# Kernel optimization log

Measured on AMD Instinct MI355X. Metric: run time of the kernel, lower is better.

Reference implementation:

```python
import math
import jax, jax.numpy as jnp
import numpy as np

NUM_EXPERTS = 8
TOP_K = 2
HIDDEN = 1024
INTERMEDIATE = 4096
CAPACITY_FACTOR = 1.0


def setup_inputs() -> dict:
    key = jax.random.key(0)
    k1, k2, k3, k4, k5, k6 = jax.random.split(key, 6)
    T = 8192
    hidden_states = jax.random.normal(k1, (T, HIDDEN), dtype=jnp.float32)
    # router affinities (already softmax-normalized in the real pipeline; uniform here is fine for correctness)
    expert_affinities = jax.random.uniform(k2, (T, NUM_EXPERTS), dtype=jnp.float32)
    expert_index = jax.random.randint(k3, (T, TOP_K), 0, NUM_EXPERTS, dtype=jnp.int32)
    scale = 0.02
    gate_w = jax.random.normal(k4, (NUM_EXPERTS, HIDDEN, INTERMEDIATE), dtype=jnp.float32) * scale
    up_w = jax.random.normal(k5, (NUM_EXPERTS, HIDDEN, INTERMEDIATE), dtype=jnp.float32) * scale
    down_w = jax.random.normal(k6, (NUM_EXPERTS, INTERMEDIATE, HIDDEN), dtype=jnp.float32) * scale
    return {"hidden_states": hidden_states, "expert_affinities": expert_affinities,
            "gate_w": gate_w, "up_w": up_w, "down_w": down_w, "expert_index": expert_index}


def reference(hidden_states, expert_affinities, gate_w, up_w, down_w, expert_index):
    T, H = hidden_states.shape
    E, K = NUM_EXPERTS, TOP_K
    C = min(math.ceil(T * K * CAPACITY_FACTOR / E), T)  # expert capacity (static)

    # top_k-hot expert mask (T, E)
    expert_mask = jax.nn.one_hot(expert_index, E, dtype=jnp.float32).sum(axis=1)
    # 1-indexed position of each token within each expert's queue
    position_in_expert = jnp.cumsum(expert_mask, axis=0)
    # capacity-based token dropping
    expert_mask = jnp.where(position_in_expert > C, 0.0, expert_mask)

    # masked (and L1-normalized) affinities of chosen experts
    aff_masked = jnp.where(expert_mask == 0, 0.0, expert_affinities)
    denom = jnp.maximum(jnp.sum(jnp.abs(aff_masked), axis=1, keepdims=True), 1e-12)
    aff_masked = aff_masked / denom  # normalize_top_k_affinities=True

    # flattened slot index per (token, expert): expert e occupies slots [e*C, (e+1)*C)
    offsets = jnp.arange(E, dtype=jnp.float32) * C
    pos_off = position_in_expert + offsets[None, :]
    pos_off = jnp.where(expert_mask == 0, 0.0, pos_off)

    # (T, K) slot index (1-based; 0 == dropped)
    perm_idx = jnp.take_along_axis(pos_off, expert_index, axis=1).astype(jnp.int32)

    # invert permutation: slot -> token (1-based; slot 0 collects all dropped tokens, then discarded)
    tok_ids = jnp.broadcast_to((jnp.arange(T, dtype=jnp.int32) + 1)[:, None], (T, K)).reshape(-1)
    assign = jnp.zeros(E * C + 1, dtype=jnp.int32).at[perm_idx.reshape(-1)].set(tok_ids)
    assign = assign[1:].reshape(E, C) - 1
    assign = jnp.maximum(assign, 0)          # empty slots read token 0 (output unused)
    perm_idx = jnp.maximum(perm_idx - 1, 0)  # dropped tokens read slot 0 (affinity == 0)

    # gather tokens into per-expert blocks and run grouped GLU MLP
    x_e = hidden_states[assign]  # (E, C, H)
    gate = jax.nn.silu(jnp.einsum('ech,ehi->eci', x_e, gate_w))
    inter = gate * jnp.einsum('ech,ehi->eci', x_e, up_w)  # (E, C, I)
    out_e = jnp.einsum('eci,eih->ech', inter, down_w)      # (E, C, H)
    permuted_output = out_e.reshape(E * C, H)

    # combine: gather each token's top_k expert outputs weighted by masked affinities
    out_k = permuted_output[perm_idx]                                   # (T, K, H)
    aff_k = jnp.take_along_axis(aff_masked, expert_index, axis=1)       # (T, K)
    return jnp.sum(out_k * aff_k[:, :, None], axis=1)
```

## Files before the change

kernel.cpp:

```cpp
#include <hip/hip_runtime.h>
#include <stdint.h>

#define T_TOK 8192
#define HID   1024
#define INTER 4096
#define NE    8
#define TOPK  2
#define CAP   2048
#define EC    (NE * CAP)


typedef __attribute__((ext_vector_type(8))) short bf16x8;
typedef __attribute__((ext_vector_type(4))) float f32x4;

static __device__ __forceinline__ unsigned short f2bf(float f) {
    union { float f; unsigned u; } a; a.f = f;
    unsigned r = a.u + 0x7FFFu + ((a.u >> 16) & 1u);
    return (unsigned short)(r >> 16);
}
static __device__ __forceinline__ float bf2f(unsigned short b) {
    union { unsigned u; float f; } a; a.u = ((unsigned)b) << 16;
    return a.f;
}

static __device__ __forceinline__ void gload(const unsigned short* g, unsigned short* l) {
    __builtin_amdgcn_global_load_lds((__attribute__((address_space(1))) void*)(uintptr_t)g,
                                     (__attribute__((address_space(3))) void*)l, 16, 0, 0);
}

#define BAR() do { asm volatile("" ::: "memory"); __builtin_amdgcn_s_barrier(); asm volatile("" ::: "memory"); } while (0)
#define WAITVM(N) asm volatile("s_waitcnt vmcnt(" #N ")" ::: "memory")

__global__ __launch_bounds__(512) void route_kernel(const int* __restrict__ eidx,
                                                    int* __restrict__ perm,
                                                    int* __restrict__ assign) {
    int tid = threadIdx.x;
    for (int i = tid; i < EC; i += 512) assign[i] = 0;
    __syncthreads();
    int e = tid >> 6;
    int lane = tid & 63;
    const int TPL = T_TOK / 64;
    int t0 = lane * TPL;
    int cnt = 0;
    for (int t = t0; t < t0 + TPL; ++t) {
        int e0 = eidx[t * 2], e1 = eidx[t * 2 + 1];
        cnt += (e0 == e) + (e1 == e);
    }
    int incl = cnt;
    #pragma unroll
    for (int off = 1; off < 64; off <<= 1) {
        int n = __shfl_up(incl, off, 64);
        if (lane >= off) incl += n;
    }
    int run = incl - cnt;
    for (int t = t0; t < t0 + TPL; ++t) {
        int e0 = eidx[t * 2], e1 = eidx[t * 2 + 1];
        int c = (e0 == e) + (e1 == e);
        if (c) {
            run += c;
            int pos = run;
            bool keep = (pos <= CAP);
            int pi = keep ? (pos + e * CAP) : 0;
            if (e0 == e) perm[t * 2]     = pi;
            if (e1 == e) perm[t * 2 + 1] = pi;
            if (keep) assign[pi - 1] = t;
        }
    }
}

__global__ __launch_bounds__(256) void transpose_cvt(const float* __restrict__ in,
                                                     unsigned short* __restrict__ out,
                                                     int R, int Cc) {
    __shared__ unsigned short tile[64][68];
    int e = blockIdx.z;
    const float* inp = in + (size_t)e * R * Cc;
    unsigned short* outp = out + (size_t)e * R * Cc;
    int c0 = blockIdx.x * 64, r0 = blockIdx.y * 64;
    int t = threadIdx.x;
    int x = t & 15;
    int ry = t >> 4;
    #pragma unroll
    for (int j = 0; j < 4; ++j) {
        int row = ry + 16 * j;
        float4 v = *(const float4*)(inp + (size_t)(r0 + row) * Cc + c0 + 4 * x);
        ushort4 o;
        o.x = f2bf(v.x); o.y = f2bf(v.y); o.z = f2bf(v.z); o.w = f2bf(v.w);
        *(ushort4*)&tile[row][4 * x] = o;
    }
    __syncthreads();
    #pragma unroll
    for (int j = 0; j < 4; ++j) {
        int oc = ry + 16 * j;
        ushort4 o;
        o.x = tile[4 * x + 0][oc];
        o.y = tile[4 * x + 1][oc];
        o.z = tile[4 * x + 2][oc];
        o.w = tile[4 * x + 3][oc];
        *(ushort4*)(outp + (size_t)(c0 + oc) * R + r0 + 4 * x) = o;
    }
}

__global__ __launch_bounds__(256) void gather_cvt(const float* __restrict__ hs,
                                                  const int* __restrict__ assign,
                                                  unsigned short* __restrict__ xe) {
    int s = blockIdx.x;
    int tok = assign[s];
    const float* src = hs + (size_t)tok * HID;
    unsigned short* dst = xe + (size_t)s * HID;
    int h = threadIdx.x * 4;
    float4 v = *(const float4*)(src + h);
    ushort4 o;
    o.x = f2bf(v.x); o.y = f2bf(v.y); o.z = f2bf(v.z); o.w = f2bf(v.w);
    *(ushort4*)(dst + h) = o;
}


__global__ __launch_bounds__(512, 2) void gateup_gemm(const unsigned short* __restrict__ Xe,
                                                      const unsigned short* __restrict__ WgT,
                                                      const unsigned short* __restrict__ WuT,
                                                      unsigned short* __restrict__ interB) {
    extern __shared__ __align__(16) unsigned short smemU[];
    const int K = HID;
    const int NT = K / 64;

    int d  = blockIdx.x + 8 * blockIdx.y + 256 * blockIdx.z;
    int e  = d & 7;
    int m0 = ((d >> 3) & 7) * 256;
    int n0 = (d >> 6) * 128;

    int tid = threadIdx.x;
    int lane = tid & 63, w = tid >> 6;
    int lm = lane & 15, hi = lane >> 4;
    int wm = w >> 2, wn = w & 3;

    const int aRd  = (wm * 128 + lm) * 32 + ((hi ^ (lm & 3)) << 3);
    const int bRd0 = (wn * 32 + lm) * 64 + ((hi ^ (lm & 7)) << 3);
    const int bRd1 = (wn * 32 + lm) * 64 + (((4 + hi) ^ (lm & 7)) << 3);

    int sAr = w * 32 + (lane >> 2);
    int sAc = ((lane & 3) ^ ((lane >> 2) & 3)) << 3;
    const unsigned short* aS0 = Xe + ((size_t)e * CAP + m0 + sAr) * K + sAc;
    const unsigned short* aS1 = aS0 + (size_t)16 * K;
    int sBr = w * 16 + (lane >> 3);
    int sBc = ((lane & 7) ^ ((lane >> 3) & 7)) << 3;
    const unsigned short* gS0 = WgT + ((size_t)e * INTER + n0 + sBr) * K + sBc;
    const unsigned short* gS1 = gS0 + (size_t)8 * K;
    const unsigned short* uS0 = WuT + ((size_t)e * INTER + n0 + sBr) * K + sBc;
    const unsigned short* uS1 = uS0 + (size_t)8 * K;

    const int dj0 = (w * 2 + 0) * 512;
    const int dj1 = (w * 2 + 1) * 512;

    f32x4 zero = {0.f, 0.f, 0.f, 0.f};
    f32x4 accG[8][2], accU[8][2];
    #pragma unroll
    for (int i = 0; i < 8; ++i) {
        accG[i][0] = zero; accG[i][1] = zero;
        accU[i][0] = zero; accU[i][1] = zero;
    }

    {
        unsigned short* wr = smemU;
        gload(aS0,      wr + dj0);          gload(aS1,      wr + dj1);
        gload(gS0,      wr + 16384 + dj0);  gload(gS1,      wr + 16384 + dj1);
        gload(uS0,      wr + 24576 + dj0);  gload(uS1,      wr + 24576 + dj1);
        gload(aS0 + 32, wr + 8192 + dj0);   gload(aS1 + 32, wr + 8192 + dj1);
        WAITVM(4);
        BAR();
    }

    bf16x8 aF[8];

    for (int t = 0; t < NT - 1; ++t) {
        const unsigned short* rd = smemU + (t & 1) * 32768;
        unsigned short* wr = smemU + ((t + 1) & 1) * 32768;
        const int gk = (t + 1) * 64;
        #pragma unroll
        for (int mi = 0; mi < 8; ++mi) aF[mi] = *(const bf16x8*)(rd + aRd + mi * 512);
        bf16x8 b0 = *(const bf16x8*)(rd + 16384 + bRd0);
        bf16x8 b1 = *(const bf16x8*)(rd + 16384 + bRd0 + 1024);
        gload(aS0 + gk, wr + dj0);          gload(aS1 + gk, wr + dj1);
        gload(gS0 + gk, wr + 16384 + dj0);  gload(gS1 + gk, wr + 16384 + dj1);
        WAITVM(6);
        BAR();
        __builtin_amdgcn_s_setprio(1);
        #pragma unroll
        for (int mi = 0; mi < 8; ++mi) {
            accG[mi][0] = __builtin_amdgcn_mfma_f32_16x16x32_bf16(aF[mi], b0, accG[mi][0], 0, 0, 0);
            accG[mi][1] = __builtin_amdgcn_mfma_f32_16x16x32_bf16(aF[mi], b1, accG[mi][1], 0, 0, 0);
        }
        __builtin_amdgcn_s_setprio(0);
        BAR();
        b0 = *(const bf16x8*)(rd + 24576 + bRd0);
        b1 = *(const bf16x8*)(rd + 24576 + bRd0 + 1024);
        gload(uS0 + gk, wr + 24576 + dj0);  gload(uS1 + gk, wr + 24576 + dj1);
        WAITVM(6);
        BAR();
        __builtin_amdgcn_s_setprio(1);
        #pragma unroll
        for (int mi = 0; mi < 8; ++mi) {
            accU[mi][0] = __builtin_amdgcn_mfma_f32_16x16x32_bf16(aF[mi], b0, accU[mi][0], 0, 0, 0);
            accU[mi][1] = __builtin_amdgcn_mfma_f32_16x16x32_bf16(aF[mi], b1, accU[mi][1], 0, 0, 0);
        }
        __builtin_amdgcn_s_setprio(0);
        BAR();
        #pragma unroll
        for (int mi = 0; mi < 8; ++mi) aF[mi] = *(const bf16x8*)(rd + 8192 + aRd + mi * 512);
        b0 = *(const bf16x8*)(rd + 16384 + bRd1);
        b1 = *(const bf16x8*)(rd + 16384 + bRd1 + 1024);
        gload(aS0 + gk + 32, wr + 8192 + dj0);  gload(aS1 + gk + 32, wr + 8192 + dj1);
        BAR();
        __builtin_amdgcn_s_setprio(1);
        #pragma unroll
        for (int mi = 0; mi < 8; ++mi) {
            accG[mi][0] = __builtin_amdgcn_mfma_f32_16x16x32_bf16(aF[mi], b0, accG[mi][0], 0, 0, 0);
            accG[mi][1] = __builtin_amdgcn_mfma_f32_16x16x32_bf16(aF[mi], b1, accG[mi][1], 0, 0, 0);
        }
        __builtin_amdgcn_s_setprio(0);
        BAR();
        b0 = *(const bf16x8*)(rd + 24576 + bRd1);
        b1 = *(const bf16x8*)(rd + 24576 + bRd1 + 1024);
        WAITVM(4);
        BAR();
        __builtin_amdgcn_s_setprio(1);
        #pragma unroll
        for (int mi = 0; mi < 8; ++mi) {
            accU[mi][0] = __builtin_amdgcn_mfma_f32_16x16x32_bf16(aF[mi], b0, accU[mi][0], 0, 0, 0);
            accU[mi][1] = __builtin_amdgcn_mfma_f32_16x16x32_bf16(aF[mi], b1, accU[mi][1], 0, 0, 0);
        }
        __builtin_amdgcn_s_setprio(0);
        BAR();
    }
    {
        const unsigned short* rd = smemU + ((NT - 1) & 1) * 32768;
        #pragma unroll
        for (int mi = 0; mi < 8; ++mi) aF[mi] = *(const bf16x8*)(rd + aRd + mi * 512);
        bf16x8 b0 = *(const bf16x8*)(rd + 16384 + bRd0);
        bf16x8 b1 = *(const bf16x8*)(rd + 16384 + bRd0 + 1024);
        WAITVM(2);
        BAR();
        #pragma unroll
        for (int mi = 0; mi < 8; ++mi) {
            accG[mi][0] = __builtin_amdgcn_mfma_f32_16x16x32_bf16(aF[mi], b0, accG[mi][0], 0, 0, 0);
            accG[mi][1] = __builtin_amdgcn_mfma_f32_16x16x32_bf16(aF[mi], b1, accG[mi][1], 0, 0, 0);
        }
        BAR();
        b0 = *(const bf16x8*)(rd + 24576 + bRd0);
        b1 = *(const bf16x8*)(rd + 24576 + bRd0 + 1024);
        WAITVM(0);
        BAR();
        #pragma unroll
        for (int mi = 0; mi < 8; ++mi) {
            accU[mi][0] = __builtin_amdgcn_mfma_f32_16x16x32_bf16(aF[mi], b0, accU[mi][0], 0, 0, 0);
            accU[mi][1] = __builtin_amdgcn_mfma_f32_16x16x32_bf16(aF[mi], b1, accU[mi][1], 0, 0, 0);
        }
        BAR();
        #pragma unroll
        for (int mi = 0; mi < 8; ++mi) aF[mi] = *(const bf16x8*)(rd + 8192 + aRd + mi * 512);
        b0 = *(const bf16x8*)(rd + 16384 + bRd1);
        b1 = *(const bf16x8*)(rd + 16384 + bRd1 + 1024);
        BAR();
        #pragma unroll
        for (int mi = 0; mi < 8; ++mi) {
            accG[mi][0] = __builtin_amdgcn_mfma_f32_16x16x32_bf16(aF[mi], b0, accG[mi][0], 0, 0, 0);
            accG[mi][1] = __builtin_amdgcn_mfma_f32_16x16x32_bf16(aF[mi], b1, accG[mi][1], 0, 0, 0);
        }
        BAR();
        b0 = *(const bf16x8*)(rd + 24576 + bRd1);
        b1 = *(const bf16x8*)(rd + 24576 + bRd1 + 1024);
        BAR();
        #pragma unroll
        for (int mi = 0; mi < 8; ++mi) {
            accU[mi][0] = __builtin_amdgcn_mfma_f32_16x16x32_bf16(aF[mi], b0, accU[mi][0], 0, 0, 0);
            accU[mi][1] = __builtin_amdgcn_mfma_f32_16x16x32_bf16(aF[mi], b1, accU[mi][1], 0, 0, 0);
        }
        BAR();
    }

    unsigned short* bounce = smemU;
    #pragma unroll
    for (int mi = 0; mi < 8; ++mi)
        #pragma unroll
        for (int nf = 0; nf < 2; ++nf) {
            f32x4 g4 = accG[mi][nf], u4 = accU[mi][nf];
            #pragma unroll
            for (int r = 0; r < 4; ++r) {
                int row = wm * 128 + mi * 16 + hi * 4 + r;
                int col = wn * 32 + nf * 16 + lm;
                float g = g4[r];
                float s = g / (1.f + __expf(-g)) * u4[r];
                bounce[row * 136 + col] = f2bf(s);
            }
        }
    __syncthreads();
    {
        unsigned short* Op = interB + ((size_t)e * CAP + m0) * INTER + n0;
        int rr = tid >> 1, cb = (tid & 1) * 64;
        #pragma unroll
        for (int j = 0; j < 8; ++j) {
            bf16x8 v = *(const bf16x8*)&bounce[rr * 136 + cb + j * 8];
            *(bf16x8*)(Op + (size_t)rr * INTER + cb + j * 8) = v;
        }
    }
}

__global__ __launch_bounds__(512, 2) void down_gemm(const unsigned short* __restrict__ interB,
                                                    const unsigned short* __restrict__ WdT,
                                                    unsigned short* __restrict__ pout) {
    extern __shared__ __align__(16) unsigned short smemU[];
    const int K = INTER;
    const int NT = K / 64;

    int d  = blockIdx.x + 8 * blockIdx.y + 32 * blockIdx.z;
    int e  = d & 7;
    int r5 = d >> 3;
    int m0 = (r5 & 7) * 256;
    int n0 = (r5 >> 3) * 256;

    int tid = threadIdx.x;
    int lane = tid & 63, w = tid >> 6;
    int lm = lane & 15, hi = lane >> 4;
    int wm = w >> 2, wn = w & 3;

    const int aRd  = (wm * 128 + lm) * 32 + ((hi ^ (lm & 3)) << 3);
    const int bRd0 = (wn * 32 + lm) * 64 + ((hi ^ (lm & 7)) << 3);
    const int bRd1 = (wn * 32 + lm) * 64 + (((4 + hi) ^ (lm & 7)) << 3);

    int sAr = w * 32 + (lane >> 2);
    int sAc = ((lane & 3) ^ ((lane >> 2) & 3)) << 3;
    const unsigned short* aS0 = interB + ((size_t)e * CAP + m0 + sAr) * K + sAc;
    const unsigned short* aS1 = aS0 + (size_t)16 * K;
    int sBr = w * 16 + (lane >> 3);
    int sBc = ((lane & 7) ^ ((lane >> 3) & 7)) << 3;
    const unsigned short* b0S0 = WdT + ((size_t)e * HID + n0 + sBr) * K + sBc;
    const unsigned short* b0S1 = b0S0 + (size_t)8 * K;
    const unsigned short* b1S0 = b0S0 + (size_t)128 * K;
    const unsigned short* b1S1 = b1S0 + (size_t)8 * K;

    const int dj0 = (w * 2 + 0) * 512;
    const int dj1 = (w * 2 + 1) * 512;

    f32x4 zero = {0.f, 0.f, 0.f, 0.f};
    f32x4 acc[8][4];
    #pragma unroll
    for (int i = 0; i < 8; ++i)
        #pragma unroll
        for (int j = 0; j < 4; ++j) acc[i][j] = zero;

    {
        unsigned short* wr = smemU;
        gload(aS0,      wr + dj0);          gload(aS1,      wr + dj1);
        gload(b0S0,     wr + 16384 + dj0);  gload(b0S1,     wr + 16384 + dj1);
        gload(b1S0,     wr + 24576 + dj0);  gload(b1S1,     wr + 24576 + dj1);
        gload(aS0 + 32, wr + 8192 + dj0);   gload(aS1 + 32, wr + 8192 + dj1);
        WAITVM(4);
        BAR();
    }

    bf16x8 aF[8];

    for (int t = 0; t < NT - 1; ++t) {
        const unsigned short* rd = smemU + (t & 1) * 32768;
        unsigned short* wr = smemU + ((t + 1) & 1) * 32768;
        const int gk = (t + 1) * 64;
        #pragma unroll
        for (int mi = 0; mi < 8; ++mi) aF[mi] = *(const bf16x8*)(rd + aRd + mi * 512);
        bf16x8 b0 = *(const bf16x8*)(rd + 16384 + bRd0);
        bf16x8 b1 = *(const bf16x8*)(rd + 16384 + bRd0 + 1024);
        gload(aS0 + gk, wr + dj0);           gload(aS1 + gk, wr + dj1);
        gload(b0S0 + gk, wr + 16384 + dj0);  gload(b0S1 + gk, wr + 16384 + dj1);
        WAITVM(6);
        BAR();
        __builtin_amdgcn_s_setprio(1);
        #pragma unroll
        for (int mi = 0; mi < 8; ++mi) {
            acc[mi][0] = __builtin_amdgcn_mfma_f32_16x16x32_bf16(aF[mi], b0, acc[mi][0], 0, 0, 0);
            acc[mi][1] = __builtin_amdgcn_mfma_f32_16x16x32_bf16(aF[mi], b1, acc[mi][1], 0, 0, 0);
        }
        __builtin_amdgcn_s_setprio(0);
        BAR();
        b0 = *(const bf16x8*)(rd + 24576 + bRd0);
        b1 = *(const bf16x8*)(rd + 24576 + bRd0 + 1024);
        gload(b1S0 + gk, wr + 24576 + dj0);  gload(b1S1 + gk, wr + 24576 + dj1);
        WAITVM(6);
        BAR();
        __builtin_amdgcn_s_setprio(1);
        #pragma unroll
        for (int mi = 0; mi < 8; ++mi) {
            acc[mi][2] = __builtin_amdgcn_mfma_f32_16x16x32_bf16(aF[mi], b0, acc[mi][2], 0, 0, 0);
            acc[mi][3] = __builtin_amdgcn_mfma_f32_16x16x32_bf16(aF[mi], b1, acc[mi][3], 0, 0, 0);
        }
        __builtin_amdgcn_s_setprio(0);
        BAR();
        #pragma unroll
        for (int mi = 0; mi < 8; ++mi) aF[mi] = *(const bf16x8*)(rd + 8192 + aRd + mi * 512);
        b0 = *(const bf16x8*)(rd + 16384 + bRd1);
        b1 = *(const bf16x8*)(rd + 16384 + bRd1 + 1024);
        gload(aS0 + gk + 32, wr + 8192 + dj0);  gload(aS1 + gk + 32, wr + 8192 + dj1);
        BAR();
        __builtin_amdgcn_s_setprio(1);
        #pragma unroll
        for (int mi = 0; mi < 8; ++mi) {
            acc[mi][0] = __builtin_amdgcn_mfma_f32_16x16x32_bf16(aF[mi], b0, acc[mi][0], 0, 0, 0);
            acc[mi][1] = __builtin_amdgcn_mfma_f32_16x16x32_bf16(aF[mi], b1, acc[mi][1], 0, 0, 0);
        }
        __builtin_amdgcn_s_setprio(0);
        BAR();
        b0 = *(const bf16x8*)(rd + 24576 + bRd1);
        b1 = *(const bf16x8*)(rd + 24576 + bRd1 + 1024);
        WAITVM(4);
        BAR();
        __builtin_amdgcn_s_setprio(1);
        #pragma unroll
        for (int mi = 0; mi < 8; ++mi) {
            acc[mi][2] = __builtin_amdgcn_mfma_f32_16x16x32_bf16(aF[mi], b0, acc[mi][2], 0, 0, 0);
            acc[mi][3] = __builtin_amdgcn_mfma_f32_16x16x32_bf16(aF[mi], b1, acc[mi][3], 0, 0, 0);
        }
        __builtin_amdgcn_s_setprio(0);
        BAR();
    }
    {
        const unsigned short* rd = smemU + ((NT - 1) & 1) * 32768;
        #pragma unroll
        for (int mi = 0; mi < 8; ++mi) aF[mi] = *(const bf16x8*)(rd + aRd + mi * 512);
        bf16x8 b0 = *(const bf16x8*)(rd + 16384 + bRd0);
        bf16x8 b1 = *(const bf16x8*)(rd + 16384 + bRd0 + 1024);
        WAITVM(2);
        BAR();
        #pragma unroll
        for (int mi = 0; mi < 8; ++mi) {
            acc[mi][0] = __builtin_amdgcn_mfma_f32_16x16x32_bf16(aF[mi], b0, acc[mi][0], 0, 0, 0);
            acc[mi][1] = __builtin_amdgcn_mfma_f32_16x16x32_bf16(aF[mi], b1, acc[mi][1], 0, 0, 0);
        }
        BAR();
        b0 = *(const bf16x8*)(rd + 24576 + bRd0);
        b1 = *(const bf16x8*)(rd + 24576 + bRd0 + 1024);
        WAITVM(0);
        BAR();
        #pragma unroll
        for (int mi = 0; mi < 8; ++mi) {
            acc[mi][2] = __builtin_amdgcn_mfma_f32_16x16x32_bf16(aF[mi], b0, acc[mi][2], 0, 0, 0);
            acc[mi][3] = __builtin_amdgcn_mfma_f32_16x16x32_bf16(aF[mi], b1, acc[mi][3], 0, 0, 0);
        }
        BAR();
        #pragma unroll
        for (int mi = 0; mi < 8; ++mi) aF[mi] = *(const bf16x8*)(rd + 8192 + aRd + mi * 512);
        b0 = *(const bf16x8*)(rd + 16384 + bRd1);
        b1 = *(const bf16x8*)(rd + 16384 + bRd1 + 1024);
        BAR();
        #pragma unroll
        for (int mi = 0; mi < 8; ++mi) {
            acc[mi][0] = __builtin_amdgcn_mfma_f32_16x16x32_bf16(aF[mi], b0, acc[mi][0], 0, 0, 0);
            acc[mi][1] = __builtin_amdgcn_mfma_f32_16x16x32_bf16(aF[mi], b1, acc[mi][1], 0, 0, 0);
        }
        BAR();
        b0 = *(const bf16x8*)(rd + 24576 + bRd1);
        b1 = *(const bf16x8*)(rd + 24576 + bRd1 + 1024);
        BAR();
        #pragma unroll
        for (int mi = 0; mi < 8; ++mi) {
            acc[mi][2] = __builtin_amdgcn_mfma_f32_16x16x32_bf16(aF[mi], b0, acc[mi][2], 0, 0, 0);
            acc[mi][3] = __builtin_amdgcn_mfma_f32_16x16x32_bf16(aF[mi], b1, acc[mi][3], 0, 0, 0);
        }
        BAR();
    }

    unsigned short* bounce = smemU;
    int rr = tid >> 1, cb = (tid & 1) * 64;
    #pragma unroll
    for (int mi = 0; mi < 8; ++mi)
        #pragma unroll
        for (int nfh = 0; nfh < 2; ++nfh) {
            f32x4 a4 = acc[mi][nfh];
            #pragma unroll
            for (int r = 0; r < 4; ++r)
                bounce[(wm * 128 + mi * 16 + hi * 4 + r) * 136 + wn * 32 + nfh * 16 + lm] = f2bf(a4[r]);
        }
    __syncthreads();
    {
        unsigned short* Op = pout + ((size_t)e * CAP + m0) * HID + n0;
        #pragma unroll
        for (int j = 0; j < 8; ++j) {
            bf16x8 v = *(const bf16x8*)&bounce[rr * 136 + cb + j * 8];
            *(bf16x8*)(Op + (size_t)rr * HID + cb + j * 8) = v;
        }
    }
    __syncthreads();
    #pragma unroll
    for (int mi = 0; mi < 8; ++mi)
        #pragma unroll
        for (int nfh = 0; nfh < 2; ++nfh) {
            f32x4 a4 = acc[mi][2 + nfh];
            #pragma unroll
            for (int r = 0; r < 4; ++r)
                bounce[(wm * 128 + mi * 16 + hi * 4 + r) * 136 + wn * 32 + nfh * 16 + lm] = f2bf(a4[r]);
        }
    __syncthreads();
    {
        unsigned short* Op = pout + ((size_t)e * CAP + m0) * HID + n0 + 128;
        #pragma unroll
        for (int j = 0; j < 8; ++j) {
            bf16x8 v = *(const bf16x8*)&bounce[rr * 136 + cb + j * 8];
            *(bf16x8*)(Op + (size_t)rr * HID + cb + j * 8) = v;
        }
    }
}

__global__ __launch_bounds__(256) void combine_kernel(const float* __restrict__ aff,
                                                      const int* __restrict__ eidx,
                                                      const int* __restrict__ perm,
                                                      const unsigned short* __restrict__ pout,
                                                      float* __restrict__ out) {
    int t = blockIdx.x;
    int e0 = eidx[t * 2], e1 = eidx[t * 2 + 1];
    int p0 = perm[t * 2], p1 = perm[t * 2 + 1];
    bool k0 = p0 > 0, k1 = p1 > 0;
    float a0 = aff[t * NE + e0], a1 = aff[t * NE + e1];
    float denom = (k0 ? fabsf(a0) : 0.f) + ((e1 != e0 && k1) ? fabsf(a1) : 0.f);
    denom = fmaxf(denom, 1e-12f);
    float w0 = k0 ? a0 / denom : 0.f;
    float w1 = k1 ? a1 / denom : 0.f;
    int s0 = k0 ? p0 - 1 : 0;
    int s1 = k1 ? p1 - 1 : 0;
    int h = threadIdx.x * 4;
    ushort4 v0 = *(const ushort4*)(pout + (size_t)s0 * HID + h);
    ushort4 v1 = *(const ushort4*)(pout + (size_t)s1 * HID + h);
    float4 o;
    o.x = w0 * bf2f(v0.x) + w1 * bf2f(v1.x);
    o.y = w0 * bf2f(v0.y) + w1 * bf2f(v1.y);
    o.z = w0 * bf2f(v0.z) + w1 * bf2f(v1.z);
    o.w = w0 * bf2f(v0.w) + w1 * bf2f(v1.w);
    *(float4*)(out + (size_t)t * HID + h) = o;
}

extern "C" void kernel_launch(void* const* d_in, const int* in_sizes, int n_in,
                              void* d_out, int out_size, void* d_ws, size_t ws_size,
                              hipStream_t stream) {
    const float* hs   = (const float*)d_in[0];
    const float* aff  = (const float*)d_in[1];
    const float* gw   = (const float*)d_in[2];
    const float* uw   = (const float*)d_in[3];
    const float* dw   = (const float*)d_in[4];
    const int*   eidx = (const int*)d_in[5];
    float* out = (float*)d_out;

    char* ws = (char*)d_ws;
    unsigned short* WgT    = (unsigned short*)(ws);
    unsigned short* WuT    = (unsigned short*)(ws + ((size_t)64  << 20));
    unsigned short* WdT    = (unsigned short*)(ws + ((size_t)128 << 20));
    unsigned short* Xe     = (unsigned short*)(ws + ((size_t)192 << 20));
    unsigned short* interB = (unsigned short*)(ws + ((size_t)224 << 20));
    unsigned short* pout   = (unsigned short*)(ws + ((size_t)352 << 20));
    int*            perm   = (int*)           (ws + ((size_t)416 << 20));
    int*            assign = perm + (T_TOK * TOPK);

    static int attr_set = 0;
    if (!attr_set) {
        (void)hipFuncSetAttribute((const void*)gateup_gemm,
                                  hipFuncAttributeMaxDynamicSharedMemorySize, 131072);
        (void)hipFuncSetAttribute((const void*)down_gemm,
                                  hipFuncAttributeMaxDynamicSharedMemorySize, 131072);
        attr_set = 1;
    }

    route_kernel<<<1, 512, 0, stream>>>(eidx, perm, assign);
    transpose_cvt<<<dim3(INTER / 64, HID / 64, NE), 256, 0, stream>>>(uw, WuT, HID, INTER);
    transpose_cvt<<<dim3(INTER / 64, HID / 64, NE), 256, 0, stream>>>(gw, WgT, HID, INTER);
    gather_cvt<<<EC, 256, 0, stream>>>(hs, assign, Xe);
    gateup_gemm<<<dim3(8, 32, 8), 512, 131072, stream>>>(Xe, WgT, WuT, interB);
    transpose_cvt<<<dim3(HID / 64, INTER / 64, NE), 256, 0, stream>>>(dw, WdT, INTER, HID);
    down_gemm<<<dim3(8, 4, 8), 512, 131072, stream>>>(interB, WdT, pout);
    combine_kernel<<<T_TOK, 256, 0, stream>>>(aff, eidx, perm, pout, out);
}
```

Measured before the change: 936.1 us.

## Restructure grouped GEMMs to 256-thread blocks with triple-buffered K=32 pipeline

Both the gate/up and down GEMMs move from 512-thread blocks with double-buffered K=64 stages to 256-thread blocks with smaller N tiles and a three-stage K=32 ring buffer. This cuts shared memory per block so more blocks can be resident, and keeps more loads in flight. The gate and up weight transposes are merged into a single launch, and the down-weight transpose moves ahead of the gate/up GEMM. In exchange, each block does more loop iterations with more barriers, and the smaller tiles give less reuse of loaded data.

```diff
diff --git a/kernel.cpp b/kernel.cpp
--- a/kernel.cpp
+++ b/kernel.cpp
@@ -68,6 +68,43 @@
     }
 }
 
+__global__ __launch_bounds__(256) void transpose_cvt2(const float* __restrict__ in0,
+                                                      unsigned short* __restrict__ out0,
+                                                      const float* __restrict__ in1,
+                                                      unsigned short* __restrict__ out1) {
+    __shared__ unsigned short tile[64][68];
+    int z = blockIdx.z;
+    const float* in = (z < 8) ? in0 : in1;
+    unsigned short* out = (z < 8) ? out0 : out1;
+    int e = z & 7;
+    const int R = HID, Cc = INTER;
+    const float* inp = in + (size_t)e * R * Cc;
+    unsigned short* outp = out + (size_t)e * R * Cc;
+    int c0 = blockIdx.x * 64, r0 = blockIdx.y * 64;
+    int t = threadIdx.x;
+    int x = t & 15;
+    int ry = t >> 4;
+    #pragma unroll
+    for (int j = 0; j < 4; ++j) {
+        int row = ry + 16 * j;
+        float4 v = *(const float4*)(inp + (size_t)(r0 + row) * Cc + c0 + 4 * x);
+        ushort4 o;
+        o.x = f2bf(v.x); o.y = f2bf(v.y); o.z = f2bf(v.z); o.w = f2bf(v.w);
+        *(ushort4*)&tile[row][4 * x] = o;
+    }
+    __syncthreads();
+    #pragma unroll
+    for (int j = 0; j < 4; ++j) {
+        int oc = ry + 16 * j;
+        ushort4 o;
+        o.x = tile[4 * x + 0][oc];
+        o.y = tile[4 * x + 1][oc];
+        o.z = tile[4 * x + 2][oc];
+        o.w = tile[4 * x + 3][oc];
+        *(ushort4*)(outp + (size_t)(c0 + oc) * R + r0 + 4 * x) = o;
+    }
+}
+
 __global__ __launch_bounds__(256) void transpose_cvt(const float* __restrict__ in,
                                                      unsigned short* __restrict__ out,
                                                      int R, int Cc) {
@@ -115,41 +152,49 @@
 }
 
 
-__global__ __launch_bounds__(512, 2) void gateup_gemm(const unsigned short* __restrict__ Xe,
+#define BUFE 12288
+
+#define MFMA16(ACC, O, B0, B1) \
+    _Pragma("unroll") \
+    for (int mi = 0; mi < 8; ++mi) { \
+        ACC[mi][O]     = __builtin_amdgcn_mfma_f32_16x16x32_bf16(aF[mi], B0, ACC[mi][O], 0, 0, 0); \
+        ACC[mi][O + 1] = __builtin_amdgcn_mfma_f32_16x16x32_bf16(aF[mi], B1, ACC[mi][O + 1], 0, 0, 0); \
+    }
+
+#define LOAD_AF(rd) \
+    _Pragma("unroll") \
+    for (int mi = 0; mi < 8; ++mi) aF[mi] = *(const bf16x8*)((rd) + aRd + mi * 512);
+
+__global__ __launch_bounds__(256, 2) void gateup_gemm(const unsigned short* __restrict__ Xe,
                                                       const unsigned short* __restrict__ WgT,
                                                       const unsigned short* __restrict__ WuT,
                                                       unsigned short* __restrict__ interB) {
     extern __shared__ __align__(16) unsigned short smemU[];
     const int K = HID;
-    const int NT = K / 64;
-
-    int d  = blockIdx.x + 8 * blockIdx.y + 256 * blockIdx.z;
-    int e  = d & 7;
-    int m0 = ((d >> 3) & 7) * 256;
-    int n0 = (d >> 6) * 128;
+    const int NT = K / 32;
+
+    int e  = blockIdx.x;
+    int m0 = blockIdx.y * 256;
+    int n0 = blockIdx.z * 64;
 
     int tid = threadIdx.x;
     int lane = tid & 63, w = tid >> 6;
     int lm = lane & 15, hi = lane >> 4;
-    int wm = w >> 2, wn = w & 3;
-
-    const int aRd  = (wm * 128 + lm) * 32 + ((hi ^ (lm & 3)) << 3);
-    const int bRd0 = (wn * 32 + lm) * 64 + ((hi ^ (lm & 7)) << 3);
-    const int bRd1 = (wn * 32 + lm) * 64 + (((4 + hi) ^ (lm & 7)) << 3);
-
-    int sAr = w * 32 + (lane >> 2);
-    int sAc = ((lane & 3) ^ ((lane >> 2) & 3)) << 3;
-    const unsigned short* aS0 = Xe + ((size_t)e * CAP + m0 + sAr) * K + sAc;
-    const unsigned short* aS1 = aS0 + (size_t)16 * K;
-    int sBr = w * 16 + (lane >> 3);
-    int sBc = ((lane & 7) ^ ((lane >> 3) & 7)) << 3;
-    const unsigned short* gS0 = WgT + ((size_t)e * INTER + n0 + sBr) * K + sBc;
-    const unsigned short* gS1 = gS0 + (size_t)8 * K;
-    const unsigned short* uS0 = WuT + ((size_t)e * INTER + n0 + sBr) * K + sBc;
-    const unsigned short* uS1 = uS0 + (size_t)8 * K;
-
-    const int dj0 = (w * 2 + 0) * 512;
-    const int dj1 = (w * 2 + 1) * 512;
+    int wm = w >> 1, wn = w & 1;
+
+    const int swz  = (hi ^ ((lm >> 1) & 3)) << 3;
+    const int aRd  = (wm * 128 + lm) * 32 + swz;
+    const int r1Rd = 8192  + (wn * 32 + lm) * 32 + swz;
+    const int r2Rd = 10240 + (wn * 32 + lm) * 32 + swz;
+
+    int sr = lane >> 2;
+    int sc = ((lane & 3) ^ ((lane >> 3) & 3)) << 3;
+    const unsigned short* aS = Xe  + ((size_t)e * CAP   + m0 + w * 64 + sr) * K + sc;
+    const unsigned short* gS = WgT + ((size_t)e * INTER + n0 + w * 16 + sr) * K + sc;
+    const unsigned short* uS = WuT + ((size_t)e * INTER + n0 + w * 16 + sr) * K + sc;
+    const int dA = w * 2048;
+    const int dG = 8192  + w * 512;
+    const int dU = 10240 + w * 512;
 
     f32x4 zero = {0.f, 0.f, 0.f, 0.f};
     f32x4 accG[8][2], accU[8][2];
@@ -159,124 +204,81 @@
         accU[i][0] = zero; accU[i][1] = zero;
     }
 
-    {
-        unsigned short* wr = smemU;
-        gload(aS0,      wr + dj0);          gload(aS1,      wr + dj1);
-        gload(gS0,      wr + 16384 + dj0);  gload(gS1,      wr + 16384 + dj1);
-        gload(uS0,      wr + 24576 + dj0);  gload(uS1,      wr + 24576 + dj1);
-        gload(aS0 + 32, wr + 8192 + dj0);   gload(aS1 + 32, wr + 8192 + dj1);
-        WAITVM(4);
+    unsigned short* p0 = smemU;
+    unsigned short* p1 = smemU + BUFE;
+    unsigned short* p2 = smemU + 2 * BUFE;
+
+    {
+        #pragma unroll
+        for (int j = 0; j < 4; ++j) gload(aS + (size_t)j * 16 * K, p0 + dA + j * 512);
+        gload(gS, p0 + dG); gload(uS, p0 + dU);
+        #pragma unroll
+        for (int j = 0; j < 4; ++j) gload(aS + (size_t)j * 16 * K + 32, p1 + dA + j * 512);
+        gload(gS + 32, p1 + dG); gload(uS + 32, p1 + dU);
+        WAITVM(7);
         BAR();
     }
 
     bf16x8 aF[8];
-
-    for (int t = 0; t < NT - 1; ++t) {
-        const unsigned short* rd = smemU + (t & 1) * 32768;
-        unsigned short* wr = smemU + ((t + 1) & 1) * 32768;
-        const int gk = (t + 1) * 64;
-        #pragma unroll
-        for (int mi = 0; mi < 8; ++mi) aF[mi] = *(const bf16x8*)(rd + aRd + mi * 512);
-        bf16x8 b0 = *(const bf16x8*)(rd + 16384 + bRd0);
-        bf16x8 b1 = *(const bf16x8*)(rd + 16384 + bRd0 + 1024);
-        gload(aS0 + gk, wr + dj0);          gload(aS1 + gk, wr + dj1);
-        gload(gS0 + gk, wr + 16384 + dj0);  gload(gS1 + gk, wr + 16384 + dj1);
+    int gk = 64;
+    for (int t = 0; t < NT - 2; ++t) {
+        const unsigned short* rd = p0;
+        unsigned short* wr = p2;
+        LOAD_AF(rd);
+        bf16x8 b0 = *(const bf16x8*)(rd + r1Rd);
+        bf16x8 b1 = *(const bf16x8*)(rd + r1Rd + 512);
+        #pragma unroll
+        for (int j = 0; j < 4; ++j) gload(aS + (size_t)j * 16 * K + gk, wr + dA + j * 512);
+        gload(gS + gk, wr + dG);
+        WAITVM(11);
+        BAR();
+        __builtin_amdgcn_s_setprio(1);
+        MFMA16(accG, 0, b0, b1);
+        __builtin_amdgcn_s_setprio(0);
+        BAR();
+        b0 = *(const bf16x8*)(rd + r2Rd);
+        b1 = *(const bf16x8*)(rd + r2Rd + 512);
+        gload(uS + gk, wr + dU);
+        WAITVM(7);
+        BAR();
+        __builtin_amdgcn_s_setprio(1);
+        MFMA16(accU, 0, b0, b1);
+        __builtin_amdgcn_s_setprio(0);
+        BAR();
+        unsigned short* tmp = p0; p0 = p1; p1 = p2; p2 = tmp;
+        gk += 32;
+    }
+    {
+        const unsigned short* rd = p0;
+        LOAD_AF(rd);
+        bf16x8 b0 = *(const bf16x8*)(rd + r1Rd);
+        bf16x8 b1 = *(const bf16x8*)(rd + r1Rd + 512);
         WAITVM(6);
         BAR();
-        __builtin_amdgcn_s_setprio(1);
-        #pragma unroll
-        for (int mi = 0; mi < 8; ++mi) {
-            accG[mi][0] = __builtin_amdgcn_mfma_f32_16x16x32_bf16(aF[mi], b0, accG[mi][0], 0, 0, 0);
-            accG[mi][1] = __builtin_amdgcn_mfma_f32_16x16x32_bf16(aF[mi], b1, accG[mi][1], 0, 0, 0);
-        }
-        __builtin_amdgcn_s_setprio(0);
-        BAR();
-        b0 = *(const bf16x8*)(rd + 24576 + bRd0);
-        b1 = *(const bf16x8*)(rd + 24576 + bRd0 + 1024);
-        gload(uS0 + gk, wr + 24576 + dj0);  gload(uS1 + gk, wr + 24576 + dj1);
-        WAITVM(6);
-        BAR();
-        __builtin_amdgcn_s_setprio(1);
-        #pragma unroll
-        for (int mi = 0; mi < 8; ++mi) {
-            accU[mi][0] = __builtin_amdgcn_mfma_f32_16x16x32_bf16(aF[mi], b0, accU[mi][0], 0, 0, 0);
-            accU[mi][1] = __builtin_amdgcn_mfma_f32_16x16x32_bf16(aF[mi], b1, accU[mi][1], 0, 0, 0);
-        }
-        __builtin_amdgcn_s_setprio(0);
-        BAR();
-        #pragma unroll
-        for (int mi = 0; mi < 8; ++mi) aF[mi] = *(const bf16x8*)(rd + 8192 + aRd + mi * 512);
-        b0 = *(const bf16x8*)(rd + 16384 + bRd1);
-        b1 = *(const bf16x8*)(rd + 16384 + bRd1 + 1024);
-        gload(aS0 + gk + 32, wr + 8192 + dj0);  gload(aS1 + gk + 32, wr + 8192 + dj1);
-        BAR();
-        __builtin_amdgcn_s_setprio(1);
-        #pragma unroll
-        for (int mi = 0; mi < 8; ++mi) {
-            accG[mi][0] = __builtin_amdgcn_mfma_f32_16x16x32_bf16(aF[mi], b0, accG[mi][0], 0, 0, 0);
-            accG[mi][1] = __builtin_amdgcn_mfma_f32_16x16x32_bf16(aF[mi], b1, accG[mi][1], 0, 0, 0);
-        }
-        __builtin_amdgcn_s_setprio(0);
-        BAR();
-        b0 = *(const bf16x8*)(rd + 24576 + bRd1);
-        b1 = *(const bf16x8*)(rd + 24576 + bRd1 + 1024);
-        WAITVM(4);
-        BAR();
-        __builtin_amdgcn_s_setprio(1);
-        #pragma unroll
-        for (int mi = 0; mi < 8; ++mi) {
-            accU[mi][0] = __builtin_amdgcn_mfma_f32_16x16x32_bf16(aF[mi], b0, accU[mi][0], 0, 0, 0);
-            accU[mi][1] = __builtin_amdgcn_mfma_f32_16x16x32_bf16(aF[mi], b1, accU[mi][1], 0, 0, 0);
-        }
-        __builtin_amdgcn_s_setprio(0);
-        BAR();
-    }
-    {
-        const unsigned short* rd = smemU + ((NT - 1) & 1) * 32768;
-        #pragma unroll
-        for (int mi = 0; mi < 8; ++mi) aF[mi] = *(const bf16x8*)(rd + aRd + mi * 512);
-        bf16x8 b0 = *(const bf16x8*)(rd + 16384 + bRd0);
-        bf16x8 b1 = *(const bf16x8*)(rd + 16384 + bRd0 + 1024);
-        WAITVM(2);
-        BAR();
-        #pragma unroll
-        for (int mi = 0; mi < 8; ++mi) {
-            accG[mi][0] = __builtin_amdgcn_mfma_f32_16x16x32_bf16(aF[mi], b0, accG[mi][0], 0, 0, 0);
-            accG[mi][1] = __builtin_amdgcn_mfma_f32_16x16x32_bf16(aF[mi], b1, accG[mi][1], 0, 0, 0);
-        }
-        BAR();
-        b0 = *(const bf16x8*)(rd + 24576 + bRd0);
-        b1 = *(const bf16x8*)(rd + 24576 + bRd0 + 1024);
+        MFMA16(accG, 0, b0, b1);
+        BAR();
+        b0 = *(const bf16x8*)(rd + r2Rd);
+        b1 = *(const bf16x8*)(rd + r2Rd + 512);
+        WAITVM(1);
+        BAR();
+        MFMA16(accU, 0, b0, b1);
+        BAR();
+    }
+    {
+        const unsigned short* rd = p1;
+        LOAD_AF(rd);
+        bf16x8 b0 = *(const bf16x8*)(rd + r1Rd);
+        bf16x8 b1 = *(const bf16x8*)(rd + r1Rd + 512);
         WAITVM(0);
         BAR();
-        #pragma unroll
-        for (int mi = 0; mi < 8; ++mi) {
-            accU[mi][0] = __builtin_amdgcn_mfma_f32_16x16x32_bf16(aF[mi], b0, accU[mi][0], 0, 0, 0);
-            accU[mi][1] = __builtin_amdgcn_mfma_f32_16x16x32_bf16(aF[mi], b1, accU[mi][1], 0, 0, 0);
-        }
-        BAR();
-        #pragma unroll
-        for (int mi = 0; mi < 8; ++mi) aF[mi] = *(const bf16x8*)(rd + 8192 + aRd + mi * 512);
-        b0 = *(const bf16x8*)(rd + 16384 + bRd1);
-        b1 = *(const bf16x8*)(rd + 16384 + bRd1 + 1024);
-        BAR();
-        #pragma unroll
-        for (int mi = 0; mi < 8; ++mi) {
-            accG[mi][0] = __builtin_amdgcn_mfma_f32_16x16x32_bf16(aF[mi], b0, accG[mi][0], 0, 0, 0);
-            accG[mi][1] = __builtin_amdgcn_mfma_f32_16x16x32_bf16(aF[mi], b1, accG[mi][1], 0, 0, 0);
-        }
-        BAR();
-        b0 = *(const bf16x8*)(rd + 24576 + bRd1);
-        b1 = *(const bf16x8*)(rd + 24576 + bRd1 + 1024);
-        BAR();
-        #pragma unroll
-        for (int mi = 0; mi < 8; ++mi) {
-            accU[mi][0] = __builtin_amdgcn_mfma_f32_16x16x32_bf16(aF[mi], b0, accU[mi][0], 0, 0, 0);
-            accU[mi][1] = __builtin_amdgcn_mfma_f32_16x16x32_bf16(aF[mi], b1, accU[mi][1], 0, 0, 0);
-        }
-        BAR();
-    }
-
+        MFMA16(accG, 0, b0, b1);
+        BAR();
+        b0 = *(const bf16x8*)(rd + r2Rd);
+        b1 = *(const bf16x8*)(rd + r2Rd + 512);
+        MFMA16(accU, 0, b0, b1);
+    }
+
+    __syncthreads();
     unsigned short* bounce = smemU;
     #pragma unroll
     for (int mi = 0; mi < 8; ++mi)
@@ -289,56 +291,52 @@
                 int col = wn * 32 + nf * 16 + lm;
                 float g = g4[r];
                 float s = g / (1.f + __expf(-g)) * u4[r];
-                bounce[row * 136 + col] = f2bf(s);
+                bounce[row * 72 + col] = f2bf(s);
             }
         }
     __syncthreads();
     {
         unsigned short* Op = interB + ((size_t)e * CAP + m0) * INTER + n0;
-        int rr = tid >> 1, cb = (tid & 1) * 64;
+        int rr = tid >> 3, cc = (tid & 7) * 8;
         #pragma unroll
         for (int j = 0; j < 8; ++j) {
-            bf16x8 v = *(const bf16x8*)&bounce[rr * 136 + cb + j * 8];
-            *(bf16x8*)(Op + (size_t)rr * INTER + cb + j * 8) = v;
+            int row = rr + 32 * j;
+            bf16x8 v = *(const bf16x8*)&bounce[row * 72 + cc];
+            *(bf16x8*)(Op + (size_t)row * INTER + cc) = v;
         }
     }
 }
 
-__global__ __launch_bounds__(512, 2) void down_gemm(const unsigned short* __restrict__ interB,
+__global__ __launch_bounds__(256, 2) void down_gemm(const unsigned short* __restrict__ interB,
                                                     const unsigned short* __restrict__ WdT,
                                                     unsigned short* __restrict__ pout) {
     extern __shared__ __align__(16) unsigned short smemU[];
     const int K = INTER;
-    const int NT = K / 64;
-
-    int d  = blockIdx.x + 8 * blockIdx.y + 32 * blockIdx.z;
-    int e  = d & 7;
-    int r5 = d >> 3;
-    int m0 = (r5 & 7) * 256;
-    int n0 = (r5 >> 3) * 256;
+    const int NT = K / 32;
+
+    int e  = blockIdx.x;
+    int m0 = blockIdx.y * 256;
+    int n0 = blockIdx.z * 128;
 
     int tid = threadIdx.x;
     int lane = tid & 63, w = tid >> 6;
     int lm = lane & 15, hi = lane >> 4;
-    int wm = w >> 2, wn = w & 3;
-
-    const int aRd  = (wm * 128 + lm) * 32 + ((hi ^ (lm & 3)) << 3);
-    const int bRd0 = (wn * 32 + lm) * 64 + ((hi ^ (lm & 7)) << 3);
-    const int bRd1 = (wn * 32 + lm) * 64 + (((4 + hi) ^ (lm & 7)) << 3);
-
-    int sAr = w * 32 + (lane >> 2);
-    int sAc = ((lane & 3) ^ ((lane >> 2) & 3)) << 3;
-    const unsigned short* aS0 = interB + ((size_t)e * CAP + m0 + sAr) * K + sAc;
-    const unsigned short* aS1 = aS0 + (size_t)16 * K;
-    int sBr = w * 16 + (lane >> 3);
-    int sBc = ((lane & 7) ^ ((lane >> 3) & 7)) << 3;
-    const unsigned short* b0S0 = WdT + ((size_t)e * HID + n0 + sBr) * K + sBc;
-    const unsigned short* b0S1 = b0S0 + (size_t)8 * K;
-    const unsigned short* b1S0 = b0S0 + (size_t)128 * K;
-    const unsigned short* b1S1 = b1S0 + (size_t)8 * K;
-
-    const int dj0 = (w * 2 + 0) * 512;
-    const int dj1 = (w * 2 + 1) * 512;
+    int wm = w >> 1, wn = w & 1;
+
+    const int swz  = (hi ^ ((lm >> 1) & 3)) << 3;
+    const int aRd  = (wm * 128 + lm) * 32 + swz;
+    const int r1Rd = 8192  + (wn * 32 + lm) * 32 + swz;
+    const int r2Rd = 10240 + (wn * 32 + lm) * 32 + swz;
+
+    int sr = lane >> 2;
+    int sc = ((lane & 3) ^ ((lane >> 3) & 3)) << 3;
+    const unsigned short* aS = interB + ((size_t)e * CAP + m0 + w * 64 + sr) * K + sc;
+    int rb1 = (w >> 1) * 64 + (w & 1) * 16;
+    const unsigned short* b1S = WdT + ((size_t)e * HID + n0 + rb1 + sr) * K + sc;
+    const unsigned short* b2S = WdT + ((size_t)e * HID + n0 + rb1 + 32 + sr) * K + sc;
+    const int dA = w * 2048;
+    const int d1 = 8192  + w * 512;
+    const int d2 = 10240 + w * 512;
 
     f32x4 zero = {0.f, 0.f, 0.f, 0.f};
     f32x4 acc[8][4];
@@ -347,161 +345,106 @@
         #pragma unroll
         for (int j = 0; j < 4; ++j) acc[i][j] = zero;
 
-    {
-        unsigned short* wr = smemU;
-        gload(aS0,      wr + dj0);          gload(aS1,      wr + dj1);
-        gload(b0S0,     wr + 16384 + dj0);  gload(b0S1,     wr + 16384 + dj1);
-        gload(b1S0,     wr + 24576 + dj0);  gload(b1S1,     wr + 24576 + dj1);
-        gload(aS0 + 32, wr + 8192 + dj0);   gload(aS1 + 32, wr + 8192 + dj1);
-        WAITVM(4);
+    unsigned short* p0 = smemU;
+    unsigned short* p1 = smemU + BUFE;
+    unsigned short* p2 = smemU + 2 * BUFE;
+
+    {
+        #pragma unroll
+        for (int j = 0; j < 4; ++j) gload(aS + (size_t)j * 16 * K, p0 + dA + j * 512);
+        gload(b1S, p0 + d1); gload(b2S, p0 + d2);
+        #pragma unroll
+        for (int j = 0; j < 4; ++j) gload(aS + (size_t)j * 16 * K + 32, p1 + dA + j * 512);
+        gload(b1S + 32, p1 + d1); gload(b2S + 32, p1 + d2);
+        WAITVM(7);
         BAR();
     }
 
     bf16x8 aF[8];
-
-    for (int t = 0; t < NT - 1; ++t) {
-        const unsigned short* rd = smemU + (t & 1) * 32768;
-        unsigned short* wr = smemU + ((t + 1) & 1) * 32768;
-        const int gk = (t + 1) * 64;
-        #pragma unroll
-        for (int mi = 0; mi < 8; ++mi) aF[mi] = *(const bf16x8*)(rd + aRd + mi * 512);
-        bf16x8 b0 = *(const bf16x8*)(rd + 16384 + bRd0);
-        bf16x8 b1 = *(const bf16x8*)(rd + 16384 + bRd0 + 1024);
-        gload(aS0 + gk, wr + dj0);           gload(aS1 + gk, wr + dj1);
-        gload(b0S0 + gk, wr + 16384 + dj0);  gload(b0S1 + gk, wr + 16384 + dj1);
+    int gk = 64;
+    for (int t = 0; t < NT - 2; ++t) {
+        const unsigned short* rd = p0;
+        unsigned short* wr = p2;
+        LOAD_AF(rd);
+        bf16x8 b0 = *(const bf16x8*)(rd + r1Rd);
+        bf16x8 b1 = *(const bf16x8*)(rd + r1Rd + 512);
+        #pragma unroll
+        for (int j = 0; j < 4; ++j) gload(aS + (size_t)j * 16 * K + gk, wr + dA + j * 512);
+        gload(b1S + gk, wr + d1);
+        WAITVM(11);
+        BAR();
+        __builtin_amdgcn_s_setprio(1);
+        MFMA16(acc, 0, b0, b1);
+        __builtin_amdgcn_s_setprio(0);
+        BAR();
+        b0 = *(const bf16x8*)(rd + r2Rd);
+        b1 = *(const bf16x8*)(rd + r2Rd + 512);
+        gload(b2S + gk, wr + d2);
+        WAITVM(7);
+        BAR();
+        __builtin_amdgcn_s_setprio(1);
+        MFMA16(acc, 2, b0, b1);
+        __builtin_amdgcn_s_setprio(0);
+        BAR();
+        unsigned short* tmp = p0; p0 = p1; p1 = p2; p2 = tmp;
+        gk += 32;
+    }
+    {
+        const unsigned short* rd = p0;
+        LOAD_AF(rd);
+        bf16x8 b0 = *(const bf16x8*)(rd + r1Rd);
+        bf16x8 b1 = *(const bf16x8*)(rd + r1Rd + 512);
         WAITVM(6);
         BAR();
-        __builtin_amdgcn_s_setprio(1);
-        #pragma unroll
-        for (int mi = 0; mi < 8; ++mi) {
-            acc[mi][0] = __builtin_amdgcn_mfma_f32_16x16x32_bf16(aF[mi], b0, acc[mi][0], 0, 0, 0);
-            acc[mi][1] = __builtin_amdgcn_mfma_f32_16x16x32_bf16(aF[mi], b1, acc[mi][1], 0, 0, 0);
-        }
-        __builtin_amdgcn_s_setprio(0);
-        BAR();
-        b0 = *(const bf16x8*)(rd + 24576 + bRd0);
-        b1 = *(const bf16x8*)(rd + 24576 + bRd0 + 1024);
-        gload(b1S0 + gk, wr + 24576 + dj0);  gload(b1S1 + gk, wr + 24576 + dj1);
-        WAITVM(6);
-        BAR();
-        __builtin_amdgcn_s_setprio(1);
-        #pragma unroll
-        for (int mi = 0; mi < 8; ++mi) {
-            acc[mi][2] = __builtin_amdgcn_mfma_f32_16x16x32_bf16(aF[mi], b0, acc[mi][2], 0, 0, 0);
-            acc[mi][3] = __builtin_amdgcn_mfma_f32_16x16x32_bf16(aF[mi], b1, acc[mi][3], 0, 0, 0);
-        }
-        __builtin_amdgcn_s_setprio(0);
-        BAR();
-        #pragma unroll
-        for (int mi = 0; mi < 8; ++mi) aF[mi] = *(const bf16x8*)(rd + 8192 + aRd + mi * 512);
-        b0 = *(const bf16x8*)(rd + 16384 + bRd1);
-        b1 = *(const bf16x8*)(rd + 16384 + bRd1 + 1024);
-        gload(aS0 + gk + 32, wr + 8192 + dj0);  gload(aS1 + gk + 32, wr + 8192 + dj1);
-        BAR();
-        __builtin_amdgcn_s_setprio(1);
-        #pragma unroll
-        for (int mi = 0; mi < 8; ++mi) {
-            acc[mi][0] = __builtin_amdgcn_mfma_f32_16x16x32_bf16(aF[mi], b0, acc[mi][0], 0, 0, 0);
-            acc[mi][1] = __builtin_amdgcn_mfma_f32_16x16x32_bf16(aF[mi], b1, acc[mi][1], 0, 0, 0);
-        }
-        __builtin_amdgcn_s_setprio(0);
-        BAR();
-        b0 = *(const bf16x8*)(rd + 24576 + bRd1);
-        b1 = *(const bf16x8*)(rd + 24576 + bRd1 + 1024);
-        WAITVM(4);
-        BAR();
-        __builtin_amdgcn_s_setprio(1);
-        #pragma unroll
-        for (int mi = 0; mi < 8; ++mi) {
-            acc[mi][2] = __builtin_amdgcn_mfma_f32_16x16x32_bf16(aF[mi], b0, acc[mi][2], 0, 0, 0);
-            acc[mi][3] = __builtin_amdgcn_mfma_f32_16x16x32_bf16(aF[mi], b1, acc[mi][3], 0, 0, 0);
-        }
-        __builtin_amdgcn_s_setprio(0);
-        BAR();
-    }
-    {
-        const unsigned short* rd = smemU + ((NT - 1) & 1) * 32768;
-        #pragma unroll
-        for (int mi = 0; mi < 8; ++mi) aF[mi] = *(const bf16x8*)(rd + aRd + mi * 512);
-        bf16x8 b0 = *(const bf16x8*)(rd + 16384 + bRd0);
-        bf16x8 b1 = *(const bf16x8*)(rd + 16384 + bRd0 + 1024);
-        WAITVM(2);
-        BAR();
-        #pragma unroll
-        for (int mi = 0; mi < 8; ++mi) {
-            acc[mi][0] = __builtin_amdgcn_mfma_f32_16x16x32_bf16(aF[mi], b0, acc[mi][0], 0, 0, 0);
-            acc[mi][1] = __builtin_amdgcn_mfma_f32_16x16x32_bf16(aF[mi], b1, acc[mi][1], 0, 0, 0);
-        }
-        BAR();
-        b0 = *(const bf16x8*)(rd + 24576 + bRd0);
-        b1 = *(const bf16x8*)(rd + 24576 + bRd0 + 1024);
+        MFMA16(acc, 0, b0, b1);
+        BAR();
+        b0 = *(const bf16x8*)(rd + r2Rd);
+        b1 = *(const bf16x8*)(rd + r2Rd + 512);
+        WAITVM(1);
+        BAR();
+        MFMA16(acc, 2, b0, b1);
+        BAR();
+    }
+    {
+        const unsigned short* rd = p1;
+        LOAD_AF(rd);
+        bf16x8 b0 = *(const bf16x8*)(rd + r1Rd);
+        bf16x8 b1 = *(const bf16x8*)(rd + r1Rd + 512);
         WAITVM(0);
         BAR();
-        #pragma unroll
-        for (int mi = 0; mi < 8; ++mi) {
-            acc[mi][2] = __builtin_amdgcn_mfma_f32_16x16x32_bf16(aF[mi], b0, acc[mi][2], 0, 0, 0);
-            acc[mi][3] = __builtin_amdgcn_mfma_f32_16x16x32_bf16(aF[mi], b1, acc[mi][3], 0, 0, 0);
-        }
-        BAR();
-        #pragma unroll
-        for (int mi = 0; mi < 8; ++mi) aF[mi] = *(const bf16x8*)(rd + 8192 + aRd + mi * 512);
-        b0 = *(const bf16x8*)(rd + 16384 + bRd1);
-        b1 = *(const bf16x8*)(rd + 16384 + bRd1 + 1024);
-        BAR();
-        #pragma unroll
-        for (int mi = 0; mi < 8; ++mi) {
-            acc[mi][0] = __builtin_amdgcn_mfma_f32_16x16x32_bf16(aF[mi], b0, acc[mi][0], 0, 0, 0);
-            acc[mi][1] = __builtin_amdgcn_mfma_f32_16x16x32_bf16(aF[mi], b1, acc[mi][1], 0, 0, 0);
-        }
-        BAR();
-        b0 = *(const bf16x8*)(rd + 24576 + bRd1);
-        b1 = *(const bf16x8*)(rd + 24576 + bRd1 + 1024);
-        BAR();
-        #pragma unroll
-        for (int mi = 0; mi < 8; ++mi) {
-            acc[mi][2] = __builtin_amdgcn_mfma_f32_16x16x32_bf16(aF[mi], b0, acc[mi][2], 0, 0, 0);
-            acc[mi][3] = __builtin_amdgcn_mfma_f32_16x16x32_bf16(aF[mi], b1, acc[mi][3], 0, 0, 0);
-        }
-        BAR();
+        MFMA16(acc, 0, b0, b1);
+        BAR();
+        b0 = *(const bf16x8*)(rd + r2Rd);
+        b1 = *(const bf16x8*)(rd + r2Rd + 512);
+        MFMA16(acc, 2, b0, b1);
     }
 
     unsigned short* bounce = smemU;
-    int rr = tid >> 1, cb = (tid & 1) * 64;
-    #pragma unroll
-    for (int mi = 0; mi < 8; ++mi)
-        #pragma unroll
-        for (int nfh = 0; nfh < 2; ++nfh) {
-            f32x4 a4 = acc[mi][nfh];
+    unsigned short* Op = pout + ((size_t)e * CAP + m0) * HID + n0;
+    int rr = tid >> 3, c8 = tid & 7;
+    int colp = c8 * 8;
+    #pragma unroll
+    for (int R = 0; R < 2; ++R) {
+        __syncthreads();
+        #pragma unroll
+        for (int mi = 0; mi < 8; ++mi)
             #pragma unroll
-            for (int r = 0; r < 4; ++r)
-                bounce[(wm * 128 + mi * 16 + hi * 4 + r) * 136 + wn * 32 + nfh * 16 + lm] = f2bf(a4[r]);
-        }
-    __syncthreads();
-    {
-        unsigned short* Op = pout + ((size_t)e * CAP + m0) * HID + n0;
+            for (int nf = 0; nf < 2; ++nf) {
+                f32x4 a4 = acc[mi][2 * R + nf];
+                #pragma unroll
+                for (int r = 0; r < 4; ++r) {
+                    int row = wm * 128 + mi * 16 + hi * 4 + r;
+                    int col = wn * 32 + nf * 16 + lm;
+                    bounce[row * 72 + col] = f2bf(a4[r]);
+                }
+            }
+        __syncthreads();
+        int gcol = (colp >> 5) * 64 + R * 32 + (colp & 31);
         #pragma unroll
         for (int j = 0; j < 8; ++j) {
-            bf16x8 v = *(const bf16x8*)&bounce[rr * 136 + cb + j * 8];
-            *(bf16x8*)(Op + (size_t)rr * HID + cb + j * 8) = v;
-        }
-    }
-    __syncthreads();
-    #pragma unroll
-    for (int mi = 0; mi < 8; ++mi)
-        #pragma unroll
-        for (int nfh = 0; nfh < 2; ++nfh) {
-            f32x4 a4 = acc[mi][2 + nfh];
-            #pragma unroll
-            for (int r = 0; r < 4; ++r)
-                bounce[(wm * 128 + mi * 16 + hi * 4 + r) * 136 + wn * 32 + nfh * 16 + lm] = f2bf(a4[r]);
-        }
-    __syncthreads();
-    {
-        unsigned short* Op = pout + ((size_t)e * CAP + m0) * HID + n0 + 128;
-        #pragma unroll
-        for (int j = 0; j < 8; ++j) {
-            bf16x8 v = *(const bf16x8*)&bounce[rr * 136 + cb + j * 8];
-            *(bf16x8*)(Op + (size_t)rr * HID + cb + j * 8) = v;
+            int row = rr + 32 * j;
+            bf16x8 v = *(const bf16x8*)&bounce[row * 72 + colp];
+            *(bf16x8*)(Op + (size_t)row * HID + gcol) = v;
         }
     }
 }
@@ -536,6 +479,7 @@
 extern "C" void kernel_launch(void* const* d_in, const int* in_sizes, int n_in,
                               void* d_out, int out_size, void* d_ws, size_t ws_size,
                               hipStream_t stream) {
+    (void)in_sizes; (void)n_in; (void)out_size; (void)ws_size;
     const float* hs   = (const float*)d_in[0];
     const float* aff  = (const float*)d_in[1];
     const float* gw   = (const float*)d_in[2];
@@ -557,18 +501,17 @@
     static int attr_set = 0;
     if (!attr_set) {
         (void)hipFuncSetAttribute((const void*)gateup_gemm,
-                                  hipFuncAttributeMaxDynamicSharedMemorySize, 131072);
+                                  hipFuncAttributeMaxDynamicSharedMemorySize, 73728);
         (void)hipFuncSetAttribute((const void*)down_gemm,
-                                  hipFuncAttributeMaxDynamicSharedMemorySize, 131072);
+                                  hipFuncAttributeMaxDynamicSharedMemorySize, 73728);
         attr_set = 1;
     }
 
     route_kernel<<<1, 512, 0, stream>>>(eidx, perm, assign);
-    transpose_cvt<<<dim3(INTER / 64, HID / 64, NE), 256, 0, stream>>>(uw, WuT, HID, INTER);
-    transpose_cvt<<<dim3(INTER / 64, HID / 64, NE), 256, 0, stream>>>(gw, WgT, HID, INTER);
+    transpose_cvt2<<<dim3(INTER / 64, HID / 64, 16), 256, 0, stream>>>(uw, WuT, gw, WgT);
+    transpose_cvt<<<dim3(HID / 64, INTER / 64, NE), 256, 0, stream>>>(dw, WdT, INTER, HID);
     gather_cvt<<<EC, 256, 0, stream>>>(hs, assign, Xe);
-    gateup_gemm<<<dim3(8, 32, 8), 512, 131072, stream>>>(Xe, WgT, WuT, interB);
-    transpose_cvt<<<dim3(HID / 64, INTER / 64, NE), 256, 0, stream>>>(dw, WdT, INTER, HID);
-    down_gemm<<<dim3(8, 4, 8), 512, 131072, stream>>>(interB, WdT, pout);
+    gateup_gemm<<<dim3(8, 8, 64), 256, 73728, stream>>>(Xe, WgT, WuT, interB);
+    down_gemm<<<dim3(8, 8, 8), 256, 73728, stream>>>(interB, WdT, pout);
     combine_kernel<<<T_TOK, 256, 0, stream>>>(aff, eidx, perm, pout, out);
 }
```

Result: faster. 912.0 us (-2.6%).
